# Optimization experiments

Measured on AMD Instinct MI355X. Metric: run time of the kernel, lower is better.

## Reference

```python
import jax, jax.numpy as jnp
import numpy as np


def _lstm_scan(x_bte, W_ih, W_hh, b_ih, b_hh, h0, c0):
    """Single-layer LSTM over time (torch gate order i,f,g,o).
    x_bte: [B,T,E]; returns (h_seq [B,T,H], (h_T, c_T))."""
    H = h0.shape[-1]
    # precompute input projections for all timesteps: [T,B,4H]
    xp = jnp.einsum('bte,ge->tbg', x_bte, W_ih) + (b_ih + b_hh)

    def step(carry, xg):
        h, c = carry
        gates = xg + h @ W_hh.T  # [B,4H]
        i, f, g, o = jnp.split(gates, 4, axis=-1)
        c = jax.nn.sigmoid(f) * c + jax.nn.sigmoid(i) * jnp.tanh(g)
        h = jax.nn.sigmoid(o) * jnp.tanh(c)
        return (h, c), h

    (hT, cT), h_seq = jax.lax.scan(step, (h0, c0), xp)
    return jnp.transpose(h_seq, (1, 0, 2)), (hT, cT)


def setup_inputs() -> dict:
    key = jax.random.key(0)
    ks = jax.random.split(key, 10)
    V, E, H = 32000, 256, 512
    B, S, T = 64, 64, 32
    s = 0.02
    return {
        'src': jax.random.randint(ks[0], (B, S), 0, V),
        'tgt': jax.random.randint(ks[1], (B, T), 0, V),
        'enc_emb': jax.random.normal(ks[2], (V, E), jnp.float32) * s,
        'dec_emb': jax.random.normal(ks[3], (V, E), jnp.float32) * s,
        'enc_Wih': jax.random.normal(ks[4], (4 * H, E), jnp.float32) * s,
        'enc_Whh': jax.random.normal(ks[5], (4 * H, H), jnp.float32) * s,
        'enc_bih': jnp.zeros((4 * H,), jnp.float32),
        'enc_bhh': jnp.zeros((4 * H,), jnp.float32),
        'dec_Wih': jax.random.normal(ks[6], (4 * H, E), jnp.float32) * s,
        'dec_Whh': jax.random.normal(ks[7], (4 * H, H), jnp.float32) * s,
        'dec_bih': jnp.zeros((4 * H,), jnp.float32),
        'dec_bhh': jnp.zeros((4 * H,), jnp.float32),
        'fc_W': jax.random.normal(ks[8], (V, H), jnp.float32) * s,
        'fc_b': jnp.zeros((V,), jnp.float32),
    }


def reference(src, tgt, enc_emb, dec_emb, enc_Wih, enc_Whh, enc_bih, enc_bhh,
              dec_Wih, dec_Whh, dec_bih, dec_bhh, fc_W, fc_b):
    B, T = tgt.shape
    H = enc_Whh.shape[-1]
    V = fc_W.shape[0]
    h0 = jnp.zeros((B, H), jnp.float32)
    c0 = jnp.zeros((B, H), jnp.float32)

    # Encoder (dropout=0.0 -> identity)
    emb_src = enc_emb[src]  # [B,S,E]
    _, (hT, cT) = _lstm_scan(emb_src, enc_Wih, enc_Whh, enc_bih, enc_bhh, h0, c0)
    hT = jax.lax.stop_gradient(hT)  # .detach() in torch source
    cT = jax.lax.stop_gradient(cT)

    # Decoder, teacher_forcing_ratio=1.0 -> inputs are tgt[:, :-1]
    emb_tgt = dec_emb[tgt[:, :-1]]  # [B,T-1,E]
    h_seq, _ = _lstm_scan(emb_tgt, dec_Wih, dec_Whh, dec_bih, dec_bhh, hT, cT)
    logits = jnp.einsum('bth,vh->btv', h_seq, fc_W) + fc_b  # [B,T-1,V]

    # outputs[:,0] stays zeros as in torch code
    outputs = jnp.concatenate([jnp.zeros((B, 1, V), jnp.float32), logits], axis=1)
    return outputs
```

## Files before the change

kernel.cpp:

```cpp
#include <hip/hip_runtime.h>
#include <cstdint>
#include <cstddef>

#define NB    64
#define SENC  64
#define TDEC  31
#define EDIM  256
#define HDIM  512
#define VOCAB 32000
#define MROWS (NB * TDEC)
#define MPAD  2048
#define NBLK  256
#define KW    32

#define HSLOT (HDIM * NB)
#define NSLOT 96

#define OFF_HH   0
#define OFF_XPE  (OFF_HH + NSLOT * HSLOT * 4)
#define OFF_XPD  (OFF_XPE + 256 * SENC * 8 * NB * 4)
#define OFF_HS   (OFF_XPD + 256 * TDEC * 8 * NB * 4)
#define OFF_FCW  (OFF_HS + MPAD * HDIM * 2)

typedef __attribute__((ext_vector_type(8))) short bf16x8;
typedef __attribute__((ext_vector_type(4))) float f32x4;

__device__ __forceinline__ float sigf(float x) { return 1.0f / (1.0f + __expf(-x)); }
__device__ __forceinline__ float tanhfast(float x) {
  return 1.0f - 2.0f / (__expf(2.0f * x) + 1.0f);
}
__device__ __forceinline__ unsigned short f2bf(float x) {
  unsigned int u = __float_as_uint(x);
  u += 0x7fffu + ((u >> 16) & 1u);
  return (unsigned short)(u >> 16);
}
__device__ __forceinline__ unsigned pack2(float a, float b) {
  return (unsigned)f2bf(a) | ((unsigned)f2bf(b) << 16);
}

__global__ __launch_bounds__(256) void setup_k(const float* __restrict__ fc_W,
                                               unsigned short* __restrict__ fcw,
                                               float* __restrict__ hh,
                                               unsigned short* __restrict__ hs,
                                               float* __restrict__ out) {
  const int gt = blockIdx.x * 256 + threadIdx.x;
  const int GSZ = 2048 * 256;
  const float4* s4 = (const float4*)fc_W;
  uint4* d4 = (uint4*)fcw;
  for (int i = gt; i < (VOCAB * HDIM / 8); i += GSZ) {
    float4 x = s4[2 * i], y = s4[2 * i + 1];
    uint4 v;
    v.x = pack2(x.x, x.y); v.y = pack2(x.z, x.w);
    v.z = pack2(y.x, y.y); v.w = pack2(y.z, y.w);
    d4[i] = v;
  }
  float4 z4 = make_float4(0.f, 0.f, 0.f, 0.f);
  for (int j = gt; j < NB * (VOCAB / 4); j += GSZ) {
    int b = j / (VOCAB / 4), q = j - b * (VOCAB / 4);
    ((float4*)out)[(size_t)b * (32 * (VOCAB / 4)) + q] = z4;
  }
  if (gt < HSLOT / 4) ((float4*)hh)[gt] = z4;
  if (gt < (MPAD - MROWS) * HDIM / 8) {
    uint4 uz = {0u, 0u, 0u, 0u};
    ((uint4*)(hs + (size_t)MROWS * HDIM))[gt] = uz;
  }
}

__device__ void xp_phase(const int* idxmat, int istride, int S,
                         const float* emb, const float* Wih,
                         const float* bih, const float* bhh,
                         float* xp_out, int bid, int tid,
                         float* W_lds, float* pbuf, float* bias_lds) {
  const int lane = tid & 63;
  const int w = tid >> 6;
  {
    int r = tid >> 5;
    int e0 = (tid & 31) * 8;
    int row_g = (r >> 1) * HDIM + bid * 2 + (r & 1);
    const float* sp = Wih + (size_t)row_g * EDIM + e0;
    *(float4*)&W_lds[r * EDIM + e0]     = *(const float4*)sp;
    *(float4*)&W_lds[r * EDIM + e0 + 4] = *(const float4*)(sp + 4);
    if (tid < 8) {
      int rg = (tid >> 1) * HDIM + bid * 2 + (tid & 1);
      bias_lds[tid] = bih[rg] + bhh[rg];
    }
  }
  __syncthreads();
  for (int s = 0; s < S; ++s) {
    int idx = idxmat[lane * istride + s];
    const float* xrow = emb + (size_t)idx * EDIM;
    float acc[8];
#pragma unroll
    for (int r = 0; r < 8; ++r) acc[r] = 0.0f;
    for (int e = w * 64; e < w * 64 + 64; e += 4) {
      float4 xv = *(const float4*)&xrow[e];
#pragma unroll
      for (int r = 0; r < 8; ++r) {
        float4 wv = *(const float4*)&W_lds[r * EDIM + e];
        acc[r] += wv.x * xv.x + wv.y * xv.y + wv.z * xv.z + wv.w * xv.w;
      }
    }
#pragma unroll
    for (int r = 0; r < 8; ++r) pbuf[(w * 8 + r) * 64 + lane] = acc[r];
    __syncthreads();
    if (tid < 128) {
      int unit = tid >> 6, b = tid & 63;
#pragma unroll
      for (int gate = 0; gate < 4; ++gate) {
        int r = gate * 2 + unit;
        float v = bias_lds[r];
#pragma unroll
        for (int ww = 0; ww < 4; ++ww) v += pbuf[(ww * 8 + r) * 64 + b];
        xp_out[((size_t)(bid * S + s) * 8 + r) * 64 + b] = v;
      }
    }
    __syncthreads();
  }
}

struct XpParams {
  const int* src; const int* tgt;
  const float* enc_emb; const float* dec_emb;
  const float* enc_Wih; const float* enc_bih; const float* enc_bhh;
  const float* dec_Wih; const float* dec_bih; const float* dec_bhh;
  float* xpe; float* xpd;
};

__global__ __launch_bounds__(256) void xp_k(XpParams p) {
  __shared__ __align__(16) float W_lds[8 * EDIM];
  __shared__ float pbuf[32 * 64];
  __shared__ float bias_lds[8];
  const int bid = blockIdx.x;
  if (bid < 256)
    xp_phase(p.src, SENC, SENC, p.enc_emb, p.enc_Wih, p.enc_bih, p.enc_bhh,
             p.xpe, bid, threadIdx.x, W_lds, pbuf, bias_lds);
  else
    xp_phase(p.tgt, 32, TDEC, p.dec_emb, p.dec_Wih, p.dec_bih, p.dec_bhh,
             p.xpd, bid - 256, threadIdx.x, W_lds, pbuf, bias_lds);
}

__device__ __forceinline__ void grid_barrier(unsigned* flags, unsigned gen) {
  asm volatile("s_waitcnt vmcnt(0)" ::: "memory");
  __syncthreads();
  const int tid = threadIdx.x;
  if (tid == 0)
    __hip_atomic_store(&flags[blockIdx.x], gen, __ATOMIC_RELAXED,
                       __HIP_MEMORY_SCOPE_AGENT);
  if (tid < 64) {
    const unsigned* f4 = flags + tid * 4;
    for (;;) {
      unsigned a = __hip_atomic_load(&f4[0], __ATOMIC_RELAXED, __HIP_MEMORY_SCOPE_AGENT);
      unsigned b = __hip_atomic_load(&f4[1], __ATOMIC_RELAXED, __HIP_MEMORY_SCOPE_AGENT);
      unsigned c = __hip_atomic_load(&f4[2], __ATOMIC_RELAXED, __HIP_MEMORY_SCOPE_AGENT);
      unsigned d = __hip_atomic_load(&f4[3], __ATOMIC_RELAXED, __HIP_MEMORY_SCOPE_AGENT);
      unsigned m0 = a < b ? a : b;
      unsigned m1 = c < d ? c : d;
      unsigned m = m0 < m1 ? m0 : m1;
      if (__all((int)(m >= gen))) break;
      __builtin_amdgcn_s_sleep(1);
    }
  }
  __syncthreads();
}

__device__ __forceinline__ void recur_phase(const float* Whh, const float* xp,
                            int S, int gen0, int last_phase, int bid, int tid,
                            float* pbuf, float* gsum, float* c_lds,
                            float* hh,
                            unsigned short* hs_or_null, unsigned* flags) {
  const int lane = tid & 63;
  const int wu = __builtin_amdgcn_readfirstlane(tid >> 6);
  const int j0 = bid * 2;

  const float* Wr[8];
#pragma unroll
  for (int r = 0; r < 8; ++r)
    Wr[r] = Whh + (size_t)((r >> 1) * HDIM + j0 + (r & 1)) * HDIM + wu * KW;

  const int unit = tid >> 6;
  const int b = tid & 63;
  float xg[4];
  if (tid < 128) {
#pragma unroll
    for (int gate = 0; gate < 4; ++gate) {
      int r = gate * 2 + unit;
      xg[gate] = xp[((size_t)(bid * S) * 8 + r) * 64 + b];
    }
  }

  for (int s = 0; s < S; ++s) {
    const float* hp = hh + (size_t)(gen0 + s) * HSLOT;
    float* hn = hh + (size_t)(gen0 + s + 1) * HSLOT;

    float hreg[KW];
    const float* hb = hp + (size_t)wu * KW * 64 + lane;
#pragma unroll
    for (int k = 0; k < KW; ++k) hreg[k] = hb[k * 64];

    float acc[8];
#pragma unroll
    for (int r = 0; r < 8; ++r) acc[r] = 0.0f;
#pragma unroll
    for (int k = 0; k < KW; ++k) {
#pragma unroll
      for (int r = 0; r < 8; ++r) acc[r] += Wr[r][k] * hreg[k];
    }
#pragma unroll
    for (int r = 0; r < 8; ++r) pbuf[(wu * 8 + r) * 64 + lane] = acc[r];
    __syncthreads();

    if (tid < 512) {
      int row = tid >> 6, bb = tid & 63;
      float v = 0.0f;
#pragma unroll
      for (int ww = 0; ww < 16; ++ww) v += pbuf[(ww * 8 + row) * 64 + bb];
      gsum[row * 64 + bb] = v;
    }
    __syncthreads();

    float xgn[4];
    if (tid < 128) {
      float g[4];
#pragma unroll
      for (int gate = 0; gate < 4; ++gate)
        g[gate] = xg[gate] + gsum[(gate * 2 + unit) * 64 + b];
      float c = c_lds[unit * 64 + b];
      float iv = sigf(g[0]), fv = sigf(g[1]);
      float gv = tanhfast(g[2]), ov = sigf(g[3]);
      c = fv * c + iv * gv;
      float h = ov * tanhfast(c);
      c_lds[unit * 64 + b] = c;
      __hip_atomic_store(&hn[(j0 + unit) * 64 + b], h, __ATOMIC_RELAXED,
                         __HIP_MEMORY_SCOPE_AGENT);
      if (hs_or_null)
        hs_or_null[((size_t)b * TDEC + s) * HDIM + j0 + unit] = f2bf(h);
      int sn = (s + 1 < S) ? s + 1 : s;
#pragma unroll
      for (int gate = 0; gate < 4; ++gate) {
        int r = gate * 2 + unit;
        xgn[gate] = xp[((size_t)(bid * S + sn) * 8 + r) * 64 + b];
      }
    }
    if (!(last_phase && s == S - 1))
      grid_barrier(flags, (unsigned)(gen0 + s + 1));
    if (tid < 128) {
#pragma unroll
      for (int gate = 0; gate < 4; ++gate) xg[gate] = xgn[gate];
    }
  }
}

struct RecurParams {
  const float* enc_Whh; const float* dec_Whh;
  const float* xpe; const float* xpd;
  float* hh;
  unsigned short* hs;
  unsigned* flags;
};

__global__ __launch_bounds__(1024, 1) void recur_coop(RecurParams p) {
  __shared__ float pbuf[128 * 64];
  __shared__ float gsum[8 * 64];
  __shared__ float c_lds[2 * 64];
  const int tid = threadIdx.x;
  const int bid = blockIdx.x;
  if (tid < 128) c_lds[tid] = 0.0f;
  __syncthreads();
  recur_phase(p.enc_Whh, p.xpe, SENC, 0, 0, bid, tid, pbuf, gsum, c_lds,
              p.hh, nullptr, p.flags);
  recur_phase(p.dec_Whh, p.xpd, TDEC, SENC, 1, bid, tid, pbuf, gsum, c_lds,
              p.hh, p.hs, p.flags);
}

__global__ __launch_bounds__(256) void fc_gemm(const unsigned short* __restrict__ A,
                                               const unsigned short* __restrict__ Bm,
                                               const float* __restrict__ bias,
                                               float* __restrict__ out) {
  __shared__ __align__(16) unsigned short As[128 * 32];
  __shared__ __align__(16) unsigned short Bs[128 * 32];
  const int tid = threadIdx.x;
  const int lane = tid & 63;
  const int w = tid >> 6;
  const int m0 = blockIdx.y * 128;
  const int n0 = blockIdx.x * 128;
  const int wm = (w >> 1) * 64;
  const int wn = (w & 1) * 64;
  const int ml = lane & 15;
  const int kq = (lane >> 4) * 8;

  f32x4 acc[4][4] = {};

  for (int k0 = 0; k0 < HDIM; k0 += 32) {
    for (int c = tid; c < 512; c += 256) {
      int row = c >> 2;
      int ko = (c & 3) * 8;
      *(uint4*)&As[c * 8] = *(const uint4*)(A + (size_t)(m0 + row) * HDIM + k0 + ko);
      *(uint4*)&Bs[c * 8] = *(const uint4*)(Bm + (size_t)(n0 + row) * HDIM + k0 + ko);
    }
    __syncthreads();
    bf16x8 fa[4], fb[4];
#pragma unroll
    for (int i = 0; i < 4; ++i)
      fa[i] = *(const bf16x8*)&As[(wm + 16 * i + ml) * 32 + kq];
#pragma unroll
    for (int j = 0; j < 4; ++j)
      fb[j] = *(const bf16x8*)&Bs[(wn + 16 * j + ml) * 32 + kq];
#pragma unroll
    for (int i = 0; i < 4; ++i)
#pragma unroll
      for (int j = 0; j < 4; ++j)
        acc[i][j] = __builtin_amdgcn_mfma_f32_16x16x32_bf16(fa[i], fb[j], acc[i][j], 0, 0, 0);
    __syncthreads();
  }

  const int rq = (lane >> 4) * 4;
#pragma unroll
  for (int j = 0; j < 4; ++j) {
    int n = n0 + wn + 16 * j + ml;
    float bv = bias[n];
#pragma unroll
    for (int i = 0; i < 4; ++i) {
#pragma unroll
      for (int r = 0; r < 4; ++r) {
        int m = m0 + wm + 16 * i + rq + r;
        if (m < MROWS) {
          int b = m / TDEC;
          int t = m - b * TDEC;
          out[((size_t)(b * 32 + t + 1)) * VOCAB + n] = acc[i][j][r] + bv;
        }
      }
    }
  }
}

extern "C" void kernel_launch(void* const* d_in, const int* in_sizes, int n_in,
                              void* d_out, int out_size, void* d_ws, size_t ws_size,
                              hipStream_t stream) {
  (void)in_sizes; (void)n_in; (void)out_size; (void)ws_size;
  const int* src      = (const int*)d_in[0];
  const int* tgt      = (const int*)d_in[1];
  const float* enc_emb = (const float*)d_in[2];
  const float* dec_emb = (const float*)d_in[3];
  const float* enc_Wih = (const float*)d_in[4];
  const float* enc_Whh = (const float*)d_in[5];
  const float* enc_bih = (const float*)d_in[6];
  const float* enc_bhh = (const float*)d_in[7];
  const float* dec_Wih = (const float*)d_in[8];
  const float* dec_Whh = (const float*)d_in[9];
  const float* dec_bih = (const float*)d_in[10];
  const float* dec_bhh = (const float*)d_in[11];
  const float* fc_W    = (const float*)d_in[12];
  const float* fc_b    = (const float*)d_in[13];
  char* ws = (char*)d_ws;
  float* hh  = (float*)(ws + OFF_HH);
  float* xpe = (float*)(ws + OFF_XPE);
  float* xpd = (float*)(ws + OFF_XPD);
  unsigned short* hs  = (unsigned short*)(ws + OFF_HS);
  unsigned short* fcw = (unsigned short*)(ws + OFF_FCW);
  unsigned* flags = (unsigned*)(ws + OFF_HS + (size_t)MROWS * HDIM * 2);
  float* out = (float*)d_out;

  hipLaunchKernelGGL(setup_k, dim3(2048), dim3(256), 0, stream, fc_W, fcw, hh, hs, out);

  XpParams xq = { src, tgt, enc_emb, dec_emb, enc_Wih, enc_bih, enc_bhh,
                  dec_Wih, dec_bih, dec_bhh, xpe, xpd };
  hipLaunchKernelGGL(xp_k, dim3(512), dim3(256), 0, stream, xq);

  RecurParams rp = { enc_Whh, dec_Whh, xpe, xpd, hh, hs, flags };
  void* args[] = { &rp };
  hipLaunchCooperativeKernel((const void*)recur_coop, dim3(NBLK), dim3(1024), args, 0, stream);

  hipLaunchKernelGGL(fc_gemm, dim3(VOCAB / 128, MPAD / 128), dim3(256), 0, stream,
                     hs, fcw, fc_b, out);
}
```

Measured before the change: 2.407 ms.

## Partition LSTM recurrence by batch groups with per-group barriers and transposed W_hh

Splits the recurrent kernel into 8 independent batch groups of 32 blocks each, so every timestep synchronises only within a group instead of across the whole grid. W_hh is transposed and gate-interleaved in the setup kernel so each lane reads coalesced weight columns, and the hidden state is read through uniform (scalar) pointers. Blocks shrink to 512 threads and the separate LDS reduction pass is folded into the gate computation. Each block now streams a 512x64 weight slice every step, which raises weight traffic per step, and the setup kernel does extra transpose work.

```diff
diff --git a/kernel.cpp b/kernel.cpp
--- a/kernel.cpp
+++ b/kernel.cpp
@@ -10,14 +10,18 @@
 #define VOCAB 32000
 #define MROWS (NB * TDEC)
 #define MPAD  2048
-#define NBLK  256
-#define KW    32
+
+#define NGRP  8
+#define GBLK  32
+#define NBLK  (NGRP * GBLK)
 
 #define HSLOT (HDIM * NB)
 #define NSLOT 96
 
 #define OFF_HH   0
-#define OFF_XPE  (OFF_HH + NSLOT * HSLOT * 4)
+#define OFF_WTE  (OFF_HH + NSLOT * HSLOT * 4)
+#define OFF_WTD  (OFF_WTE + 2048 * 512 * 4)
+#define OFF_XPE  (OFF_WTD + 2048 * 512 * 4)
 #define OFF_XPD  (OFF_XPE + 256 * SENC * 8 * NB * 4)
 #define OFF_HS   (OFF_XPD + 256 * TDEC * 8 * NB * 4)
 #define OFF_FCW  (OFF_HS + MPAD * HDIM * 2)
@@ -37,9 +41,19 @@
 __device__ __forceinline__ unsigned pack2(float a, float b) {
   return (unsigned)f2bf(a) | ((unsigned)f2bf(b) << 16);
 }
+__device__ __forceinline__ const float* uni(const float* p) {
+  uintptr_t a = (uintptr_t)p;
+  unsigned lo = __builtin_amdgcn_readfirstlane((unsigned)a);
+  unsigned hi = __builtin_amdgcn_readfirstlane((unsigned)(a >> 32));
+  return (const float*)(((uintptr_t)hi << 32) | lo);
+}
 
 __global__ __launch_bounds__(256) void setup_k(const float* __restrict__ fc_W,
+                                               const float* __restrict__ eW,
+                                               const float* __restrict__ dW,
                                                unsigned short* __restrict__ fcw,
+                                               float* __restrict__ wte,
+                                               float* __restrict__ wtd,
                                                float* __restrict__ hh,
                                                unsigned short* __restrict__ hs,
                                                float* __restrict__ out) {
@@ -53,6 +67,13 @@
     v.x = pack2(x.x, x.y); v.y = pack2(x.z, x.w);
     v.z = pack2(y.x, y.y); v.w = pack2(y.z, y.w);
     d4[i] = v;
+  }
+  for (int i = gt; i < 2048 * 512; i += GSZ) {
+    int row = i >> 9, k = i & 511;
+    int gate = row >> 9, u = row & 511;
+    int pos = (u >> 4) * 64 + gate * 16 + (u & 15);
+    wte[(size_t)k * 2048 + pos] = eW[i];
+    wtd[(size_t)k * 2048 + pos] = dW[i];
   }
   float4 z4 = make_float4(0.f, 0.f, 0.f, 0.f);
   for (int j = gt; j < NB * (VOCAB / 4); j += GSZ) {
@@ -139,110 +160,95 @@
              p.xpd, bid - 256, threadIdx.x, W_lds, pbuf, bias_lds);
 }
 
-__device__ __forceinline__ void grid_barrier(unsigned* flags, unsigned gen) {
+__device__ __forceinline__ void group_barrier(unsigned* fg, int wid, unsigned gen) {
   asm volatile("s_waitcnt vmcnt(0)" ::: "memory");
   __syncthreads();
-  const int tid = threadIdx.x;
-  if (tid == 0)
-    __hip_atomic_store(&flags[blockIdx.x], gen, __ATOMIC_RELAXED,
-                       __HIP_MEMORY_SCOPE_AGENT);
-  if (tid < 64) {
-    const unsigned* f4 = flags + tid * 4;
+  if (threadIdx.x == 0)
+    __hip_atomic_store(&fg[wid], gen, __ATOMIC_RELAXED, __HIP_MEMORY_SCOPE_AGENT);
+  if (threadIdx.x < 64) {
     for (;;) {
-      unsigned a = __hip_atomic_load(&f4[0], __ATOMIC_RELAXED, __HIP_MEMORY_SCOPE_AGENT);
-      unsigned b = __hip_atomic_load(&f4[1], __ATOMIC_RELAXED, __HIP_MEMORY_SCOPE_AGENT);
-      unsigned c = __hip_atomic_load(&f4[2], __ATOMIC_RELAXED, __HIP_MEMORY_SCOPE_AGENT);
-      unsigned d = __hip_atomic_load(&f4[3], __ATOMIC_RELAXED, __HIP_MEMORY_SCOPE_AGENT);
-      unsigned m0 = a < b ? a : b;
-      unsigned m1 = c < d ? c : d;
-      unsigned m = m0 < m1 ? m0 : m1;
-      if (__all((int)(m >= gen))) break;
+      unsigned v = 0xffffffffu;
+      if (threadIdx.x < GBLK)
+        v = __hip_atomic_load(&fg[threadIdx.x], __ATOMIC_RELAXED,
+                              __HIP_MEMORY_SCOPE_AGENT);
+      if (__all((int)(v >= gen))) break;
       __builtin_amdgcn_s_sleep(1);
     }
   }
   __syncthreads();
 }
 
-__device__ __forceinline__ void recur_phase(const float* Whh, const float* xp,
-                            int S, int gen0, int last_phase, int bid, int tid,
-                            float* pbuf, float* gsum, float* c_lds,
-                            float* hh,
-                            unsigned short* hs_or_null, unsigned* flags) {
+__device__ __forceinline__ void recur_phase(const float* __restrict__ WTP,
+                            const float* xp, int S, int gen0, int last_phase,
+                            int gr, int wid, int tid,
+                            float* pbuf, float* c_lds, float* hh,
+                            unsigned short* hs_or_null, unsigned* fg) {
   const int lane = tid & 63;
   const int wu = __builtin_amdgcn_readfirstlane(tid >> 6);
-  const int j0 = bid * 2;
-
-  const float* Wr[8];
-#pragma unroll
-  for (int r = 0; r < 8; ++r)
-    Wr[r] = Whh + (size_t)((r >> 1) * HDIM + j0 + (r & 1)) * HDIM + wu * KW;
-
-  const int unit = tid >> 6;
-  const int b = tid & 63;
+  const int u0 = wid * 16;
+  const int b0 = gr * 8;
+  const float* wcol = WTP + (size_t)(wu * 64) * 2048 + wid * 64 + lane;
+
+  const int b = tid & 7, uoff = tid >> 3;
+  const int u = u0 + uoff;
   float xg[4];
   if (tid < 128) {
+    int bid2 = u >> 1;
 #pragma unroll
     for (int gate = 0; gate < 4; ++gate) {
-      int r = gate * 2 + unit;
-      xg[gate] = xp[((size_t)(bid * S) * 8 + r) * 64 + b];
+      int r = gate * 2 + (u & 1);
+      xg[gate] = xp[((size_t)(bid2 * S) * 8 + r) * 64 + (b0 + b)];
     }
   }
 
   for (int s = 0; s < S; ++s) {
-    const float* hp = hh + (size_t)(gen0 + s) * HSLOT;
-    float* hn = hh + (size_t)(gen0 + s + 1) * HSLOT;
-
-    float hreg[KW];
-    const float* hb = hp + (size_t)wu * KW * 64 + lane;
-#pragma unroll
-    for (int k = 0; k < KW; ++k) hreg[k] = hb[k * 64];
-
-    float acc[8];
-#pragma unroll
-    for (int r = 0; r < 8; ++r) acc[r] = 0.0f;
-#pragma unroll
-    for (int k = 0; k < KW; ++k) {
-#pragma unroll
-      for (int r = 0; r < 8; ++r) acc[r] += Wr[r][k] * hreg[k];
-    }
-#pragma unroll
-    for (int r = 0; r < 8; ++r) pbuf[(wu * 8 + r) * 64 + lane] = acc[r];
-    __syncthreads();
-
-    if (tid < 512) {
-      int row = tid >> 6, bb = tid & 63;
-      float v = 0.0f;
-#pragma unroll
-      for (int ww = 0; ww < 16; ++ww) v += pbuf[(ww * 8 + row) * 64 + bb];
-      gsum[row * 64 + bb] = v;
-    }
+    const int gen = gen0 + s;
+    const float* hsec = uni(hh + ((size_t)gen * 8 + gr) * 4096 + wu * 512);
+    float acc[8] = {0.f, 0.f, 0.f, 0.f, 0.f, 0.f, 0.f, 0.f};
+#pragma unroll
+    for (int j = 0; j < 64; ++j) {
+      float wv = wcol[(size_t)j * 2048];
+#pragma unroll
+      for (int bb = 0; bb < 8; ++bb)
+        acc[bb] += wv * hsec[j * 8 + bb];
+    }
+#pragma unroll
+    for (int bb = 0; bb < 8; ++bb)
+      pbuf[(wu * 8 + bb) * 64 + lane] = acc[bb];
     __syncthreads();
 
     float xgn[4];
     if (tid < 128) {
-      float g[4];
-#pragma unroll
-      for (int gate = 0; gate < 4; ++gate)
-        g[gate] = xg[gate] + gsum[(gate * 2 + unit) * 64 + b];
-      float c = c_lds[unit * 64 + b];
-      float iv = sigf(g[0]), fv = sigf(g[1]);
-      float gv = tanhfast(g[2]), ov = sigf(g[3]);
+      float g4[4];
+#pragma unroll
+      for (int gate = 0; gate < 4; ++gate) {
+        float v = xg[gate];
+#pragma unroll
+        for (int w = 0; w < 8; ++w)
+          v += pbuf[(w * 8 + b) * 64 + gate * 16 + uoff];
+        g4[gate] = v;
+      }
+      float c = c_lds[tid];
+      float iv = sigf(g4[0]), fv = sigf(g4[1]);
+      float gv = tanhfast(g4[2]), ov = sigf(g4[3]);
       c = fv * c + iv * gv;
       float h = ov * tanhfast(c);
-      c_lds[unit * 64 + b] = c;
-      __hip_atomic_store(&hn[(j0 + unit) * 64 + b], h, __ATOMIC_RELAXED,
+      c_lds[tid] = c;
+      float* hn = hh + ((size_t)(gen + 1) * 8 + gr) * 4096;
+      __hip_atomic_store(&hn[u0 * 8 + tid], h, __ATOMIC_RELAXED,
                          __HIP_MEMORY_SCOPE_AGENT);
       if (hs_or_null)
-        hs_or_null[((size_t)b * TDEC + s) * HDIM + j0 + unit] = f2bf(h);
+        hs_or_null[((size_t)(b0 + b) * TDEC + s) * HDIM + u] = f2bf(h);
       int sn = (s + 1 < S) ? s + 1 : s;
+      int bid2 = u >> 1;
 #pragma unroll
       for (int gate = 0; gate < 4; ++gate) {
-        int r = gate * 2 + unit;
-        xgn[gate] = xp[((size_t)(bid * S + sn) * 8 + r) * 64 + b];
+        int r = gate * 2 + (u & 1);
+        xgn[gate] = xp[((size_t)(bid2 * S + sn) * 8 + r) * 64 + (b0 + b)];
       }
     }
     if (!(last_phase && s == S - 1))
-      grid_barrier(flags, (unsigned)(gen0 + s + 1));
+      group_barrier(fg, wid, (unsigned)(gen + 1));
     if (tid < 128) {
 #pragma unroll
       for (int gate = 0; gate < 4; ++gate) xg[gate] = xgn[gate];
@@ -251,25 +257,26 @@
 }
 
 struct RecurParams {
-  const float* enc_Whh; const float* dec_Whh;
+  const float* wte; const float* wtd;
   const float* xpe; const float* xpd;
   float* hh;
   unsigned short* hs;
   unsigned* flags;
 };
 
-__global__ __launch_bounds__(1024, 1) void recur_coop(RecurParams p) {
-  __shared__ float pbuf[128 * 64];
-  __shared__ float gsum[8 * 64];
-  __shared__ float c_lds[2 * 64];
+__global__ __launch_bounds__(512, 1) void recur_coop(RecurParams p) {
+  __shared__ float pbuf[64 * 64];
+  __shared__ float c_lds[128];
   const int tid = threadIdx.x;
-  const int bid = blockIdx.x;
+  const int gr = blockIdx.x & 7;
+  const int wid = blockIdx.x >> 3;
   if (tid < 128) c_lds[tid] = 0.0f;
   __syncthreads();
-  recur_phase(p.enc_Whh, p.xpe, SENC, 0, 0, bid, tid, pbuf, gsum, c_lds,
-              p.hh, nullptr, p.flags);
-  recur_phase(p.dec_Whh, p.xpd, TDEC, SENC, 1, bid, tid, pbuf, gsum, c_lds,
-              p.hh, p.hs, p.flags);
+  unsigned* fg = p.flags + gr * GBLK;
+  recur_phase(p.wte, p.xpe, SENC, 0, 0, gr, wid, tid, pbuf, c_lds,
+              p.hh, nullptr, fg);
+  recur_phase(p.wtd, p.xpd, TDEC, SENC, 1, gr, wid, tid, pbuf, c_lds,
+              p.hh, p.hs, fg);
 }
 
 __global__ __launch_bounds__(256) void fc_gemm(const unsigned short* __restrict__ A,
@@ -353,6 +360,8 @@
   const float* fc_b    = (const float*)d_in[13];
   char* ws = (char*)d_ws;
   float* hh  = (float*)(ws + OFF_HH);
+  float* wte = (float*)(ws + OFF_WTE);
+  float* wtd = (float*)(ws + OFF_WTD);
   float* xpe = (float*)(ws + OFF_XPE);
   float* xpd = (float*)(ws + OFF_XPD);
   unsigned short* hs  = (unsigned short*)(ws + OFF_HS);
@@ -360,15 +369,16 @@
   unsigned* flags = (unsigned*)(ws + OFF_HS + (size_t)MROWS * HDIM * 2);
   float* out = (float*)d_out;
 
-  hipLaunchKernelGGL(setup_k, dim3(2048), dim3(256), 0, stream, fc_W, fcw, hh, hs, out);
+  hipLaunchKernelGGL(setup_k, dim3(2048), dim3(256), 0, stream,
+                     fc_W, enc_Whh, dec_Whh, fcw, wte, wtd, hh, hs, out);
 
   XpParams xq = { src, tgt, enc_emb, dec_emb, enc_Wih, enc_bih, enc_bhh,
                   dec_Wih, dec_bih, dec_bhh, xpe, xpd };
   hipLaunchKernelGGL(xp_k, dim3(512), dim3(256), 0, stream, xq);
 
-  RecurParams rp = { enc_Whh, dec_Whh, xpe, xpd, hh, hs, flags };
+  RecurParams rp = { wte, wtd, xpe, xpd, hh, hs, flags };
   void* args[] = { &rp };
-  hipLaunchCooperativeKernel((const void*)recur_coop, dim3(NBLK), dim3(1024), args, 0, stream);
+  hipLaunchCooperativeKernel((const void*)recur_coop, dim3(NBLK), dim3(512), args, 0, stream);
 
   hipLaunchKernelGGL(fc_gemm, dim3(VOCAB / 128, MPAD / 128), dim3(256), 0, stream,
                      hs, fcw, fc_b, out);
```

Result: faster. 2.229 ms (-7.4%).
